# Optimization experiments

Measured on AMD Instinct MI355X. Metric: run time of the kernel, lower is better.

## Reference

```python
import jax, jax.numpy as jnp
import numpy as np

B, T, D, H = 128, 365, 32, 512


def setup_inputs() -> dict:
    key = jax.random.key(0)
    k_x, k_wx, k_wh, k_b = jax.random.split(key, 4)
    scale_x = 1.0 / np.sqrt(D)
    scale_h = 1.0 / np.sqrt(H)
    x = jax.random.normal(k_x, (B, T, D), dtype=jnp.float32)
    Wx = jax.random.normal(k_wx, (D, 4 * H), dtype=jnp.float32) * scale_x  # kernel, gate order i,f,g,o
    Wh = jax.random.normal(k_wh, (H, 4 * H), dtype=jnp.float32) * scale_h  # recurrent kernel
    b = jax.random.normal(k_b, (4 * H,), dtype=jnp.float32) * 0.01
    # Keras unit_forget_bias: forget-gate bias initialized to 1
    b = b.at[H:2 * H].add(1.0)
    return {"x": x, "Wx": Wx, "Wh": Wh, "b": b}


def _lstm_seq(x, Wx, Wh, b):
    # Precompute input projections for all timesteps: [B,T,4H]
    xW = jnp.einsum("btd,dg->btg", x, Wx) + b
    h0 = jnp.zeros((x.shape[0], H), dtype=x.dtype)
    c0 = jnp.zeros((x.shape[0], H), dtype=x.dtype)

    def step(carry, xw_t):
        h, c = carry
        z = xw_t + h @ Wh  # [B,4H]
        i = jax.nn.sigmoid(z[:, 0 * H:1 * H])
        f = jax.nn.sigmoid(z[:, 1 * H:2 * H])
        g = jnp.tanh(z[:, 2 * H:3 * H])
        o = jax.nn.sigmoid(z[:, 3 * H:4 * H])
        c_new = f * c + i * g
        h_new = o * jnp.tanh(c_new)
        return (h_new, c_new), h_new

    (_, _), hs = jax.lax.scan(step, (h0, c0), jnp.swapaxes(xW, 0, 1))  # hs: [T,B,H]
    return jnp.swapaxes(hs, 0, 1)  # [B,T,H]


def reference(x, Wx, Wh, b):
    # Dense layer output is discarded in the original call(); return h sequence.
    return _lstm_seq(x, Wx, Wh, b)
```

## Files before the change

### kernel.cpp

```cpp
#include <hip/hip_runtime.h>
#include <hip/hip_fp16.h>
#include <cmath>

#define BB 128
#define TT 365
#define DD 32
#define HH 512
#define G4H 2048


typedef float f32x4 __attribute__((ext_vector_type(4)));
typedef _Float16 f16x8 __attribute__((ext_vector_type(8)));

__device__ __forceinline__ float sigf(float z) { return 1.f / (1.f + __expf(-z)); }

__global__ __launch_bounds__(512, 2)
void lstm_persistent(const float* __restrict__ x,
                     const float* __restrict__ Wx,
                     const float* __restrict__ Wh,
                     const float* __restrict__ bias,
                     float* __restrict__ out,
                     float* __restrict__ hws) {
  __shared__ __align__(16) _Float16 WlH[128 * 552];
  __shared__ __align__(16) _Float16 AshH[8 * 552];
  __shared__ __align__(16) float ZxS[8 * 128];
  __shared__ __align__(16) float Cs[8][32];
  __shared__ __align__(16) float BiasS[128];

  const int tid = threadIdx.x;
  const int lane = tid & 63;
  const int wv = tid >> 6;
  const int fcol = wv * 16 + (lane & 15);
  const int kq = lane >> 4;
  const int arow = lane & 15;
  const int wg = blockIdx.x;
  const int bb = wg & 15;
  const int nb = wg >> 4;
  const int b0g = bb * 8;
  const int n0 = nb * 32;

  {
    const int cl = tid & 31;
    const int pg = tid >> 5;
    for (int it = 0; it < 136; ++it) {
      int p = it * 16 + pg;
      int k = p >> 2, g = p & 3;
      int col = g * HH + n0 + cl;
      float v = (k < DD) ? Wx[k * G4H + col] : Wh[(k - DD) * G4H + col];
      WlH[(g * 32 + cl) * 552 + k] = (_Float16)v;
    }
  }
  if (tid < 128) BiasS[tid] = bias[(tid >> 5) * HH + n0 + (tid & 31)];
  if (tid < 256) Cs[tid >> 5][tid & 31] = 0.f;

  _Float16* hb0 = (_Float16*)hws;
  _Float16* hb1 = (_Float16*)(hws + BB * HH);
  unsigned int* bar = (unsigned int*)(hws + 2 * BB * HH) + bb * 32;

  __syncthreads();

  f16x8 bfrag[17];
#pragma unroll
  for (int kk = 0; kk < 17; ++kk)
    bfrag[kk] = *(const f16x8*)&WlH[fcol * 552 + kk * 32 + kq * 8];

  for (int t = 0; t < TT; ++t) {
    const _Float16* hprev = (t & 1) ? hb1 : hb0;
    _Float16* hnext = (t & 1) ? hb0 : hb1;

    if (tid < 256) {
      int r = tid >> 5, c = tid & 31;
      AshH[r * 552 + c] = (_Float16)x[((size_t)(b0g + r) * TT + t) * DD + c];
    }
    unsigned long long pre[2];
#pragma unroll
    for (int r = 0; r < 2; ++r) {
      int idx = r * 512 + tid;
      int rr = idx >> 7, kk = idx & 127;
      pre[r] = __hip_atomic_load(
          (const unsigned long long*)(hprev + (size_t)(b0g + rr) * HH + kk * 4),
          __ATOMIC_RELAXED, __HIP_MEMORY_SCOPE_AGENT);
    }
#pragma unroll
    for (int r = 0; r < 2; ++r) {
      int idx = r * 512 + tid;
      int rr = idx >> 7, kk = idx & 127;
      *(unsigned long long*)&AshH[rr * 552 + DD + kk * 4] = pre[r];
    }
    __syncthreads();

    f32x4 acc = {0.f, 0.f, 0.f, 0.f};
#pragma unroll
    for (int kk = 0; kk < 17; ++kk) {
      f16x8 af;
      if (arow < 8) {
        af = *(const f16x8*)&AshH[arow * 552 + kk * 32 + kq * 8];
      } else {
        f16x8 z = {};
        af = z;
      }
      acc = __builtin_amdgcn_mfma_f32_16x16x32_f16(af, bfrag[kk], acc, 0, 0, 0);
    }
    if (kq < 2) {
#pragma unroll
      for (int r = 0; r < 4; ++r)
        ZxS[(kq * 4 + r) * 128 + fcol] = acc[r] + BiasS[fcol];
    }
    __syncthreads();

    float hv = 0.f;
    int bg = 0, col = 0;
    if (tid < 256) {
      int b_l = tid >> 5, nn = tid & 31;
      float zi = ZxS[b_l * 128 + nn];
      float zf = ZxS[b_l * 128 + 32 + nn];
      float zg = ZxS[b_l * 128 + 64 + nn];
      float zo = ZxS[b_l * 128 + 96 + nn];
      float cnew = sigf(zf) * Cs[b_l][nn] + sigf(zi) * tanhf(zg);
      Cs[b_l][nn] = cnew;
      hv = sigf(zo) * tanhf(cnew);
      bg = b0g + b_l;
      col = n0 + nn;
      int base = lane & ~3;
      float h0 = __shfl(hv, base + 0);
      float h1 = __shfl(hv, base + 1);
      float h2 = __shfl(hv, base + 2);
      float h3 = __shfl(hv, base + 3);
      if ((lane & 3) == 0) {
        union { unsigned long long u; _Float16 h[4]; } pk;
        pk.h[0] = (_Float16)h0;
        pk.h[1] = (_Float16)h1;
        pk.h[2] = (_Float16)h2;
        pk.h[3] = (_Float16)h3;
        __hip_atomic_store(
            (unsigned long long*)(hnext + (size_t)bg * HH + col), pk.u,
            __ATOMIC_RELAXED, __HIP_MEMORY_SCOPE_AGENT);
      }
    }
    __syncthreads();

    if (tid == 0) {
      __hip_atomic_fetch_add(bar, 1u, __ATOMIC_RELAXED,
                             __HIP_MEMORY_SCOPE_AGENT);
    }
    if (tid < 256) {
      out[((size_t)bg * TT + t) * HH + col] = hv;
    }
    if (tid == 0) {
      unsigned int target = 16u * (unsigned)(t + 1);
      while (__hip_atomic_load(bar, __ATOMIC_RELAXED,
                               __HIP_MEMORY_SCOPE_AGENT) < target) {
      }
    }
    __syncthreads();
  }
}

__global__ __launch_bounds__(256, 2)
void lstm_step(const float* __restrict__ x, const float* __restrict__ Wx,
               const float* __restrict__ Wh, const float* __restrict__ bias,
               float* __restrict__ out, const float* __restrict__ hprev,
               float* __restrict__ hnext, float* __restrict__ cst, int t) {
  __shared__ float Wl[16 * 544];
  __shared__ float Ash[32 * 128];
  __shared__ float Xs[32 * 32];
  __shared__ float Zx[4][32][4];
  __shared__ float BiasS[16];

  const int tid = threadIdx.x;
  const int ks = tid & 7;
  const int btile = (tid >> 3) & 7;
  const int ctile = tid >> 6;
  const int wg = blockIdx.x;
  const int bb = wg & 3;
  const int nb = wg >> 2;
  const int b0g = bb * 32;
  const int n0 = nb * 4;

  for (int idx = tid; idx < 16 * 544; idx += 256) {
    int zc = idx & 15, k = idx >> 4;
    int col = (zc >> 2) * HH + n0 + (zc & 3);
    Wl[zc * 544 + k] = (k < DD) ? Wx[k * G4H + col] : Wh[(k - DD) * G4H + col];
  }
  if (tid < 16) BiasS[tid] = bias[(tid >> 2) * HH + n0 + (tid & 3)];

  {
    int b_l = tid >> 3, kq = tid & 7;
    float4 v = *(const float4*)(x + ((size_t)(b0g + b_l) * TT + t) * DD + kq * 4);
    *(float4*)&Xs[b_l * 32 + kq * 4] = v;
  }

  float acc[4][4];
#pragma unroll
  for (int i = 0; i < 4; ++i)
#pragma unroll
    for (int c = 0; c < 4; ++c) acc[i][c] = 0.f;

  auto mac4 = [&](const float* Abase, int rstride, const float* Wbase) {
    float4 a4[4], w4[4];
#pragma unroll
    for (int i = 0; i < 4; ++i)
      a4[i] = *(const float4*)(Abase + (btile * 4 + i) * rstride);
#pragma unroll
    for (int c = 0; c < 4; ++c) w4[c] = *(const float4*)(Wbase + c * 544);
#pragma unroll
    for (int i = 0; i < 4; ++i)
#pragma unroll
      for (int c = 0; c < 4; ++c)
        acc[i][c] += a4[i].x * w4[c].x + a4[i].y * w4[c].y +
                     a4[i].z * w4[c].z + a4[i].w * w4[c].w;
  };

  for (int ch = 0; ch < 4; ++ch) {
    __syncthreads();
    for (int r = 0; r < 4; ++r) {
      int fidx = r * 256 + tid;
      int b_l = fidx >> 5, kq = fidx & 31;
      float4 v = *(const float4*)(hprev + (size_t)(b0g + b_l) * HH + ch * 128 +
                                  kq * 4);
      *(float4*)&Ash[b_l * 128 + kq * 4] = v;
    }
    __syncthreads();
    if (ch == 0) mac4(&Xs[ks * 4], 32, &Wl[(ctile * 4) * 544 + ks * 4]);
#pragma unroll
    for (int j = 0; j < 4; ++j)
      mac4(&Ash[j * 32 + ks * 4], 128,
           &Wl[(ctile * 4) * 544 + DD + ch * 128 + j * 32 + ks * 4]);
  }

#pragma unroll
  for (int i = 0; i < 4; ++i)
#pragma unroll
    for (int c = 0; c < 4; ++c) {
      float v = acc[i][c];
      v += __shfl_xor(v, 1);
      v += __shfl_xor(v, 2);
      v += __shfl_xor(v, 4);
      acc[i][c] = v;
    }

  if (ks == 0) {
#pragma unroll
    for (int i = 0; i < 4; ++i)
#pragma unroll
      for (int c = 0; c < 4; ++c)
        Zx[ctile][btile * 4 + i][c] = acc[i][c] + BiasS[ctile * 4 + c];
  }
  __syncthreads();

  if (tid < 128) {
    int b_l = tid >> 2, nn = tid & 3;
    float zi = Zx[0][b_l][nn], zf = Zx[1][b_l][nn];
    float zg = Zx[2][b_l][nn], zo = Zx[3][b_l][nn];
    int bg = b0g + b_l, col = n0 + nn;
    size_t cidx = (size_t)bg * HH + col;
    float cnew = sigf(zf) * cst[cidx] + sigf(zi) * tanhf(zg);
    cst[cidx] = cnew;
    float hv = sigf(zo) * tanhf(cnew);
    hnext[cidx] = hv;
    out[((size_t)bg * TT + t) * HH + col] = hv;
  }
}

extern "C" void kernel_launch(void* const* d_in, const int* in_sizes, int n_in,
                              void* d_out, int out_size, void* d_ws, size_t ws_size,
                              hipStream_t stream) {
  const float* x = (const float*)d_in[0];
  const float* Wx = (const float*)d_in[1];
  const float* Wh = (const float*)d_in[2];
  const float* bv = (const float*)d_in[3];
  float* out = (float*)d_out;
  float* hws = (float*)d_ws;

  hipMemsetAsync(d_ws, 0, (size_t)(3 * 65536 + 256) * 4, stream);

  void* args[] = {(void*)&x, (void*)&Wx, (void*)&Wh,
                  (void*)&bv, (void*)&out, (void*)&hws};
  hipError_t err = hipLaunchCooperativeKernel(
      reinterpret_cast<void*>(lstm_persistent), dim3(256), dim3(512), args, 0,
      stream);
  if (err != hipSuccess) {
    (void)hipGetLastError();
    float* buf0 = hws;
    float* buf1 = hws + BB * HH;
    float* cst = hws + 2 * BB * HH + 256;
    for (int t = 0; t < TT; ++t) {
      const float* hp = (t & 1) ? buf1 : buf0;
      float* hn = (t & 1) ? buf0 : buf1;
      lstm_step<<<dim3(512), dim3(256), 0, stream>>>(x, Wx, Wh, bv, out, hp, hn,
                                                     cst, t);
    }
  }
}
```

Measured before the change: 1.086 ms.

## Replace per-step block barrier with per-wave spin and prefetch next input

```diff
diff --git a/kernel.cpp b/kernel.cpp
--- a/kernel.cpp
+++ b/kernel.cpp
@@ -13,6 +13,13 @@
 typedef _Float16 f16x8 __attribute__((ext_vector_type(8)));
 
 __device__ __forceinline__ float sigf(float z) { return 1.f / (1.f + __expf(-z)); }
+
+__device__ __forceinline__ float ftanh(float z) {
+  float a = fabsf(z);
+  float e = __expf(-2.f * a);
+  float r = (1.f - e) / (1.f + e);
+  return (z < 0.f) ? -r : r;
+}
 
 __global__ __launch_bounds__(512, 2)
 void lstm_persistent(const float* __restrict__ x,
@@ -63,15 +70,29 @@
 #pragma unroll
   for (int kk = 0; kk < 17; ++kk)
     bfrag[kk] = *(const f16x8*)&WlH[fcol * 552 + kk * 32 + kq * 8];
+  const float bias_r = BiasS[fcol];
+
+  if (tid < 256) {
+    int r = tid >> 5, c = tid & 31;
+    AshH[r * 552 + c] = (_Float16)x[((size_t)(b0g + r) * TT + 0) * DD + c];
+  }
 
   for (int t = 0; t < TT; ++t) {
     const _Float16* hprev = (t & 1) ? hb1 : hb0;
     _Float16* hnext = (t & 1) ? hb0 : hb1;
 
-    if (tid < 256) {
-      int r = tid >> 5, c = tid & 31;
-      AshH[r * 552 + c] = (_Float16)x[((size_t)(b0g + r) * TT + t) * DD + c];
-    }
+    if (t > 0) {
+      unsigned target = 16u * (unsigned)t;
+      unsigned cur;
+      do {
+        unsigned v = 0;
+        if (lane == 0)
+          v = __hip_atomic_load(bar, __ATOMIC_RELAXED,
+                                __HIP_MEMORY_SCOPE_AGENT);
+        cur = (unsigned)__shfl((int)v, 0);
+      } while (cur < target);
+    }
+
     unsigned long long pre[2];
 #pragma unroll
     for (int r = 0; r < 2; ++r) {
@@ -89,7 +110,8 @@
     }
     __syncthreads();
 
-    f32x4 acc = {0.f, 0.f, 0.f, 0.f};
+    f32x4 acc0 = {bias_r, bias_r, bias_r, bias_r};
+    f32x4 acc1 = {0.f, 0.f, 0.f, 0.f};
 #pragma unroll
     for (int kk = 0; kk < 17; ++kk) {
       f16x8 af;
@@ -99,12 +121,15 @@
         f16x8 z = {};
         af = z;
       }
-      acc = __builtin_amdgcn_mfma_f32_16x16x32_f16(af, bfrag[kk], acc, 0, 0, 0);
+      if (kk & 1)
+        acc1 = __builtin_amdgcn_mfma_f32_16x16x32_f16(af, bfrag[kk], acc1, 0, 0, 0);
+      else
+        acc0 = __builtin_amdgcn_mfma_f32_16x16x32_f16(af, bfrag[kk], acc0, 0, 0, 0);
     }
     if (kq < 2) {
 #pragma unroll
       for (int r = 0; r < 4; ++r)
-        ZxS[(kq * 4 + r) * 128 + fcol] = acc[r] + BiasS[fcol];
+        ZxS[(kq * 4 + r) * 128 + fcol] = acc0[r] + acc1[r];
     }
     __syncthreads();
 
@@ -116,9 +141,9 @@
       float zf = ZxS[b_l * 128 + 32 + nn];
       float zg = ZxS[b_l * 128 + 64 + nn];
       float zo = ZxS[b_l * 128 + 96 + nn];
-      float cnew = sigf(zf) * Cs[b_l][nn] + sigf(zi) * tanhf(zg);
+      float cnew = sigf(zf) * Cs[b_l][nn] + sigf(zi) * ftanh(zg);
       Cs[b_l][nn] = cnew;
-      hv = sigf(zo) * tanhf(cnew);
+      hv = sigf(zo) * ftanh(cnew);
       bg = b0g + b_l;
       col = n0 + nn;
       int base = lane & ~3;
@@ -137,6 +162,11 @@
             __ATOMIC_RELAXED, __HIP_MEMORY_SCOPE_AGENT);
       }
     }
+    if (t + 1 < TT && tid < 256) {
+      int r = tid >> 5, c = tid & 31;
+      AshH[r * 552 + c] =
+          (_Float16)x[((size_t)(b0g + r) * TT + (t + 1)) * DD + c];
+    }
     __syncthreads();
 
     if (tid == 0) {
@@ -146,13 +176,6 @@
     if (tid < 256) {
       out[((size_t)bg * TT + t) * HH + col] = hv;
     }
-    if (tid == 0) {
-      unsigned int target = 16u * (unsigned)(t + 1);
-      while (__hip_atomic_load(bar, __ATOMIC_RELAXED,
-                               __HIP_MEMORY_SCOPE_AGENT) < target) {
-      }
-    }
-    __syncthreads();
   }
 }
 
```

Result: no change. 1.098 ms (+1.1%).

## Repartition persistent LSTM to 4 batch rows by 64 hidden units per block

Applied to the files above, without the earlier changes.

```diff
diff --git a/kernel.cpp b/kernel.cpp
--- a/kernel.cpp
+++ b/kernel.cpp
@@ -13,6 +13,13 @@
 typedef _Float16 f16x8 __attribute__((ext_vector_type(8)));
 
 __device__ __forceinline__ float sigf(float z) { return 1.f / (1.f + __expf(-z)); }
+
+__device__ __forceinline__ float ftanh(float z) {
+  float a = fabsf(z);
+  float e = __expf(-2.f * a);
+  float r = (1.f - e) / (1.f + e);
+  return (z < 0.f) ? -r : r;
+}
 
 __global__ __launch_bounds__(512, 2)
 void lstm_persistent(const float* __restrict__ x,
@@ -22,105 +29,118 @@
                      float* __restrict__ out,
                      float* __restrict__ hws) {
   __shared__ __align__(16) _Float16 WlH[128 * 552];
-  __shared__ __align__(16) _Float16 AshH[8 * 552];
-  __shared__ __align__(16) float ZxS[8 * 128];
-  __shared__ __align__(16) float Cs[8][32];
-  __shared__ __align__(16) float BiasS[128];
+  __shared__ __align__(16) _Float16 AshH[4 * 552];
+  __shared__ __align__(16) float ZxS[4 * 256];
+  __shared__ __align__(16) float Cs[4][64];
+  __shared__ __align__(16) float BiasS[256];
 
   const int tid = threadIdx.x;
   const int lane = tid & 63;
   const int wv = tid >> 6;
-  const int fcol = wv * 16 + (lane & 15);
   const int kq = lane >> 4;
   const int arow = lane & 15;
   const int wg = blockIdx.x;
-  const int bb = wg & 15;
-  const int nb = wg >> 4;
-  const int b0g = bb * 8;
-  const int n0 = nb * 32;
-
-  {
-    const int cl = tid & 31;
-    const int pg = tid >> 5;
+  const int bb = wg & 31;
+  const int nb = wg >> 5;
+  const int b0g = bb * 4;
+  const int n0 = nb * 64;
+  const int lc0 = wv * 16 + (lane & 15);
+
+  _Float16* hb0 = (_Float16*)hws;
+  _Float16* hb1 = (_Float16*)(hws + BB * HH);
+  unsigned int* bar = (unsigned int*)(hws + 2 * BB * HH) + bb * 8;
+
+  f16x8 bfrag0[17], bfrag1[17];
+#pragma unroll 1
+  for (int p = 0; p < 2; ++p) {
+    const int cl = tid & 63;
+    const int pg = tid >> 6;
     for (int it = 0; it < 136; ++it) {
-      int p = it * 16 + pg;
-      int k = p >> 2, g = p & 3;
+      int pr = it * 8 + pg;
+      int k = pr >> 1, g_loc = pr & 1;
+      int g = p * 2 + g_loc;
       int col = g * HH + n0 + cl;
       float v = (k < DD) ? Wx[k * G4H + col] : Wh[(k - DD) * G4H + col];
-      WlH[(g * 32 + cl) * 552 + k] = (_Float16)v;
-    }
-  }
-  if (tid < 128) BiasS[tid] = bias[(tid >> 5) * HH + n0 + (tid & 31)];
-  if (tid < 256) Cs[tid >> 5][tid & 31] = 0.f;
-
-  _Float16* hb0 = (_Float16*)hws;
-  _Float16* hb1 = (_Float16*)(hws + BB * HH);
-  unsigned int* bar = (unsigned int*)(hws + 2 * BB * HH) + bb * 32;
-
+      WlH[(g_loc * 64 + cl) * 552 + k] = (_Float16)v;
+    }
+    __syncthreads();
+    if (p == 0) {
+#pragma unroll
+      for (int kk = 0; kk < 17; ++kk)
+        bfrag0[kk] = *(const f16x8*)&WlH[lc0 * 552 + kk * 32 + kq * 8];
+    } else {
+#pragma unroll
+      for (int kk = 0; kk < 17; ++kk)
+        bfrag1[kk] = *(const f16x8*)&WlH[lc0 * 552 + kk * 32 + kq * 8];
+    }
+    __syncthreads();
+  }
+  if (tid < 256) {
+    BiasS[tid] = bias[(tid >> 6) * HH + n0 + (tid & 63)];
+    Cs[tid >> 6][tid & 63] = 0.f;
+  }
   __syncthreads();
-
-  f16x8 bfrag[17];
-#pragma unroll
-  for (int kk = 0; kk < 17; ++kk)
-    bfrag[kk] = *(const f16x8*)&WlH[fcol * 552 + kk * 32 + kq * 8];
+  const float bias0 = BiasS[lc0];
+  const float bias1 = BiasS[128 + lc0];
+
+  const int rr0 = tid >> 7, kk0 = tid & 127;
 
   for (int t = 0; t < TT; ++t) {
     const _Float16* hprev = (t & 1) ? hb1 : hb0;
     _Float16* hnext = (t & 1) ? hb0 : hb1;
 
-    if (tid < 256) {
+    if (tid < 128) {
       int r = tid >> 5, c = tid & 31;
       AshH[r * 552 + c] = (_Float16)x[((size_t)(b0g + r) * TT + t) * DD + c];
     }
-    unsigned long long pre[2];
-#pragma unroll
-    for (int r = 0; r < 2; ++r) {
-      int idx = r * 512 + tid;
-      int rr = idx >> 7, kk = idx & 127;
-      pre[r] = __hip_atomic_load(
-          (const unsigned long long*)(hprev + (size_t)(b0g + rr) * HH + kk * 4),
+    {
+      unsigned long long w0 = __hip_atomic_load(
+          (const unsigned long long*)(hprev + (size_t)(b0g + rr0) * HH + kk0 * 4),
           __ATOMIC_RELAXED, __HIP_MEMORY_SCOPE_AGENT);
-    }
-#pragma unroll
-    for (int r = 0; r < 2; ++r) {
-      int idx = r * 512 + tid;
-      int rr = idx >> 7, kk = idx & 127;
-      *(unsigned long long*)&AshH[rr * 552 + DD + kk * 4] = pre[r];
-    }
-    __syncthreads();
-
-    f32x4 acc = {0.f, 0.f, 0.f, 0.f};
+      *(unsigned long long*)&AshH[rr0 * 552 + DD + kk0 * 4] = w0;
+    }
+    __syncthreads();
+
+    f32x4 a00 = {bias0, bias0, bias0, bias0};
+    f32x4 a01 = {0.f, 0.f, 0.f, 0.f};
+    f32x4 a10 = {bias1, bias1, bias1, bias1};
+    f32x4 a11 = {0.f, 0.f, 0.f, 0.f};
 #pragma unroll
     for (int kk = 0; kk < 17; ++kk) {
       f16x8 af;
-      if (arow < 8) {
+      if (arow < 4) {
         af = *(const f16x8*)&AshH[arow * 552 + kk * 32 + kq * 8];
       } else {
         f16x8 z = {};
         af = z;
       }
-      acc = __builtin_amdgcn_mfma_f32_16x16x32_f16(af, bfrag[kk], acc, 0, 0, 0);
-    }
-    if (kq < 2) {
-#pragma unroll
-      for (int r = 0; r < 4; ++r)
-        ZxS[(kq * 4 + r) * 128 + fcol] = acc[r] + BiasS[fcol];
-    }
-    __syncthreads();
-
-    float hv = 0.f;
-    int bg = 0, col = 0;
+      if (kk & 1) {
+        a01 = __builtin_amdgcn_mfma_f32_16x16x32_f16(af, bfrag0[kk], a01, 0, 0, 0);
+        a11 = __builtin_amdgcn_mfma_f32_16x16x32_f16(af, bfrag1[kk], a11, 0, 0, 0);
+      } else {
+        a00 = __builtin_amdgcn_mfma_f32_16x16x32_f16(af, bfrag0[kk], a00, 0, 0, 0);
+        a10 = __builtin_amdgcn_mfma_f32_16x16x32_f16(af, bfrag1[kk], a10, 0, 0, 0);
+      }
+    }
+    if (kq == 0) {
+#pragma unroll
+      for (int r = 0; r < 4; ++r) {
+        ZxS[r * 256 + lc0] = a00[r] + a01[r];
+        ZxS[r * 256 + 128 + lc0] = a10[r] + a11[r];
+      }
+    }
+    __syncthreads();
+
     if (tid < 256) {
-      int b_l = tid >> 5, nn = tid & 31;
-      float zi = ZxS[b_l * 128 + nn];
-      float zf = ZxS[b_l * 128 + 32 + nn];
-      float zg = ZxS[b_l * 128 + 64 + nn];
-      float zo = ZxS[b_l * 128 + 96 + nn];
-      float cnew = sigf(zf) * Cs[b_l][nn] + sigf(zi) * tanhf(zg);
+      int b_l = tid >> 6, nn = tid & 63;
+      float zi = ZxS[b_l * 256 + nn];
+      float zf = ZxS[b_l * 256 + 64 + nn];
+      float zg = ZxS[b_l * 256 + 128 + nn];
+      float zo = ZxS[b_l * 256 + 192 + nn];
+      float cnew = sigf(zf) * Cs[b_l][nn] + sigf(zi) * ftanh(zg);
       Cs[b_l][nn] = cnew;
-      hv = sigf(zo) * tanhf(cnew);
-      bg = b0g + b_l;
-      col = n0 + nn;
+      float hv = sigf(zo) * ftanh(cnew);
+      int bg = b0g + b_l, col = n0 + nn;
       int base = lane & ~3;
       float h0 = __shfl(hv, base + 0);
       float h1 = __shfl(hv, base + 1);
@@ -136,18 +156,14 @@
             (unsigned long long*)(hnext + (size_t)bg * HH + col), pk.u,
             __ATOMIC_RELAXED, __HIP_MEMORY_SCOPE_AGENT);
       }
+      __builtin_nontemporal_store(hv, &out[((size_t)bg * TT + t) * HH + col]);
     }
     __syncthreads();
 
     if (tid == 0) {
       __hip_atomic_fetch_add(bar, 1u, __ATOMIC_RELAXED,
                              __HIP_MEMORY_SCOPE_AGENT);
-    }
-    if (tid < 256) {
-      out[((size_t)bg * TT + t) * HH + col] = hv;
-    }
-    if (tid == 0) {
-      unsigned int target = 16u * (unsigned)(t + 1);
+      unsigned int target = 8u * (unsigned)(t + 1);
       while (__hip_atomic_load(bar, __ATOMIC_RELAXED,
                                __HIP_MEMORY_SCOPE_AGENT) < target) {
       }
```

Result: slower. 1.136 ms (+4.6%).
